# Kernel tuning notes

Measured on AMD Instinct MI355X. Metric: run time of the kernel, lower is better.

Reference implementation:

```python
import jax, jax.numpy as jnp
import numpy as np

NH = 8          # attention heads
TEMP = 2.0      # gumbel temperature


def _gumbel_softmax_hard(logits, key, temperature):
    # hard=True straight-through gumbel softmax (module is in eval mode)
    g = jax.random.gumbel(key, logits.shape, logits.dtype)
    y = jax.nn.softmax((logits + g) / temperature, axis=-1)
    y_hard = jax.nn.one_hot(jnp.argmax(y, axis=-1), logits.shape[-1], dtype=y.dtype)
    return y_hard - jax.lax.stop_gradient(y) + y


def _experts(x, w1, w2, w3):
    # SwiGLU FFN over all experts at once: x [T,C], w1/w3 [E,H,C], w2 [E,C,H] -> [T,E,C]
    h = jax.nn.silu(jnp.einsum('tc,ehc->teh', x, w1)) * jnp.einsum('tc,ehc->teh', x, w3)
    return jnp.einsum('teh,ech->tec', h, w2)


def _mha(q_in, kv_in, in_w, in_b, out_w, out_b):
    C = q_in.shape[-1]
    hd = C // NH
    q = q_in @ in_w[:C].T + in_b[:C]
    k = kv_in @ in_w[C:2 * C].T + in_b[C:2 * C]
    v = kv_in @ in_w[2 * C:].T + in_b[2 * C:]
    B, Tq, _ = q.shape
    Tk = k.shape[1]
    q = q.reshape(B, Tq, NH, hd)
    k = k.reshape(B, Tk, NH, hd)
    v = v.reshape(B, Tk, NH, hd)
    scale = jnp.asarray(1.0 / np.sqrt(hd), q.dtype)
    att = jax.nn.softmax(jnp.einsum('bqhd,bkhd->bhqk', q, k) * scale, axis=-1)
    o = jnp.einsum('bhqk,bkhd->bqhd', att, v).reshape(B, Tq, C)
    return o @ out_w.T + out_b


def setup_inputs() -> dict:
    key = jax.random.key(0)
    ks = jax.random.split(key, 20)
    B, T, S, C, E, H = 2, 2048, 77, 1024, 4, 2816
    p = lambda k, sh: jax.random.normal(k, sh, jnp.float32) * 0.02
    return {
        'x': jax.random.normal(ks[0], (B, T, C), jnp.float32),
        'time': jax.random.normal(ks[1], (B,), jnp.float32),
        'caption': jax.random.normal(ks[2], (B, S, C), jnp.float32),
        'language': jax.random.randint(ks[3], (B,), 0, 9),
        'lang_embed': p(ks[4], (9, C)),
        'lang_gate_w': p(ks[5], (E, C)),
        'lang_gate_b': jnp.zeros((E,), jnp.float32),
        'lang_w1': p(ks[6], (E, H, C)),
        'lang_w2': p(ks[7], (E, C, H)),
        'lang_w3': p(ks[8], (E, H, C)),
        'in_proj_w': p(ks[9], (3 * C, C)),
        'in_proj_b': jnp.zeros((3 * C,), jnp.float32),
        'out_proj_w': p(ks[10], (C, C)),
        'out_proj_b': jnp.zeros((C,), jnp.float32),
        'cap_gate_w': p(ks[11], (E, C)),
        'cap_gate_b': jnp.zeros((E,), jnp.float32),
        'cap_w1': p(ks[12], (E, H, C)),
        'cap_w2': p(ks[13], (E, C, H)),
        'cap_w3': p(ks[14], (E, H, C)),
    }


def reference(x, time, caption, language, lang_embed, lang_gate_w, lang_gate_b,
              lang_w1, lang_w2, lang_w3, in_proj_w, in_proj_b, out_proj_w, out_proj_b,
              cap_gate_w, cap_gate_b, cap_w1, cap_w2, cap_w3):
    B, T, C = x.shape
    x_flat = x.reshape(-1, C)                                   # [B*T, C]

    # language gating (one logit vector per batch element, repeated over T tokens)
    lang_emb = lang_embed[language]                             # [B, C]
    lang_logits = lang_emb @ lang_gate_w.T + lang_gate_b        # [B, E]
    lang_probs = _gumbel_softmax_hard(lang_logits, jax.random.key(1), TEMP)
    lang_probs = jnp.repeat(lang_probs, T, axis=0)              # [B*T, E]

    lang_outputs = _experts(x_flat, lang_w1, lang_w2, lang_w3)  # [B*T, E, C]
    first_out = (lang_outputs * lang_probs[:, :, None]).sum(axis=1)  # [B*T, C]
    first_reshaped = first_out.reshape(B, T, C)

    # cross attention against caption, then per-token caption gating
    cross = _mha(first_reshaped, caption, in_proj_w, in_proj_b, out_proj_w, out_proj_b)
    cross_flat = cross.reshape(-1, C)
    cap_logits = cross_flat @ cap_gate_w.T + cap_gate_b         # [B*T, E]
    cap_probs = _gumbel_softmax_hard(cap_logits, jax.random.key(2), TEMP)

    cap_outputs = _experts(first_out, cap_w1, cap_w2, cap_w3)   # [B*T, E, C]
    second_out = (cap_outputs * cap_probs[:, :, None]).sum(axis=1)

    total_out = (first_out + second_out).reshape(B, T, C)

    all_probs = jnp.concatenate([lang_probs, cap_probs], axis=1)  # [B*T, 2E]
    expert_usage = all_probs.mean(axis=0)
    loss = (expert_usage * jnp.log(expert_usage + 1e-10)).sum()
    return total_out, loss
```

## Files before the change

### kernel.cpp

```cpp
#include <hip/hip_runtime.h>
#include <stdint.h>

#define B_ 2
#define T_ 2048
#define S_ 77
#define C_ 1024
#define E_ 4
#define H_ 2816
#define NH_ 8
#define HD_ 128
#define N_ (B_*T_)
#define MAXGB (N_/128 + E_)
#define MAXGB2 (N_/256 + E_)
#define PEsz ((size_t)H_*C_)
#define CC_ ((size_t)C_*C_)

typedef _Float16 h8 __attribute__((ext_vector_type(8)));
typedef _Float16 h4 __attribute__((ext_vector_type(4)));
typedef float f4 __attribute__((ext_vector_type(4)));

__device__ __forceinline__ void gload16(const void* g, void* l){
  __builtin_amdgcn_global_load_lds((const __attribute__((address_space(1))) void*)g,
                                   (__attribute__((address_space(3))) void*)l, 16, 0, 0);
}

__device__ __forceinline__ uint32_t rotl32(uint32_t v, int r){ return (v<<r)|(v>>(32-r)); }
__device__ __forceinline__ void threefry2x32(uint32_t k0, uint32_t k1,
                                             uint32_t x, uint32_t y,
                                             uint32_t& o0, uint32_t& o1){
  uint32_t k2 = k0 ^ k1 ^ 0x1BD11BDAu;
  x += k0; y += k1;
#define TFR(r) { x += y; y = rotl32(y, r); y ^= x; }
  TFR(13) TFR(15) TFR(26) TFR(6)   x += k1; y += k2 + 1u;
  TFR(17) TFR(29) TFR(16) TFR(24)  x += k2; y += k0 + 2u;
  TFR(13) TFR(15) TFR(26) TFR(6)   x += k0; y += k1 + 3u;
  TFR(17) TFR(29) TFR(16) TFR(24)  x += k1; y += k2 + 4u;
  TFR(13) TFR(15) TFR(26) TFR(6)   x += k2; y += k0 + 5u;
#undef TFR
  o0 = x; o1 = y;
}
__device__ __forceinline__ float gumbel_from_bits(uint32_t bits){
  const float TINY = 1.17549435e-38f;
  float f = __uint_as_float((bits >> 9) | 0x3f800000u) - 1.0f;
  float u = fmaxf(TINY, f + TINY);
  return -logf(-logf(u));
}
__device__ __forceinline__ float jax_gumbel(uint32_t k0, uint32_t k1, uint32_t idx){
  uint32_t a, b;
  threefry2x32(k0, k1, 0u, idx, a, b);
  return gumbel_from_bits(a ^ b);
}

__device__ __forceinline__ void job_split(const float* __restrict__ s,
    _Float16* __restrict__ hi, _Float16* __restrict__ lo, long n4, long gtid, long gstride){
  for (long i = gtid; i < n4; i += gstride){
    float4 v = ((const float4*)s)[i];
    h4 h, L;
    h[0]=(_Float16)v.x; h[1]=(_Float16)v.y; h[2]=(_Float16)v.z; h[3]=(_Float16)v.w;
    L[0]=(_Float16)(v.x-(float)h[0]); L[1]=(_Float16)(v.y-(float)h[1]);
    L[2]=(_Float16)(v.z-(float)h[2]); L[3]=(_Float16)(v.w-(float)h[3]);
    ((h4*)hi)[i] = h; ((h4*)lo)[i] = L;
  }
}
__device__ __forceinline__ void job_plain(const float* __restrict__ s,
    _Float16* __restrict__ d, long n4, long gtid, long gstride){
  for (long i = gtid; i < n4; i += gstride){
    float4 v = ((const float4*)s)[i];
    h4 h;
    h[0]=(_Float16)v.x; h[1]=(_Float16)v.y; h[2]=(_Float16)v.z; h[3]=(_Float16)v.w;
    ((h4*)d)[i] = h;
  }
}
__device__ __forceinline__ void job_w13_plain(const float* __restrict__ w1,
    const float* __restrict__ w3, _Float16* __restrict__ dst, int nslot, long gtid, long gstride){
  const int K8 = C_/8;
  long total = (long)nslot * (2*H_) * K8;
  for (long i = gtid; i < total; i += gstride){
    int kv = (int)(i & (K8-1));
    long rs = i >> 7;
    int r  = (int)(rs % (2*H_));
    int slot = (int)(rs / (2*H_));
    int gg = r >> 5, o = r & 31;
    const float* src = ((o<16)? w1 : w3) + (size_t)slot*PEsz + (size_t)(16*gg + (o&15))*C_ + kv*8;
    float4 v0 = *(const float4*)src, v1 = *(const float4*)(src+4);
    float vv[8] = {v0.x,v0.y,v0.z,v0.w,v1.x,v1.y,v1.z,v1.w};
    h8 hh;
#pragma unroll
    for (int jj=0;jj<8;++jj) hh[jj] = (_Float16)vv[jj];
    *(h8*)(dst + (size_t)slot*2*PEsz + (size_t)r*C_ + kv*8) = hh;
  }
}
__device__ __forceinline__ void job_w13_split_sel(const float* __restrict__ w1,
    const float* __restrict__ w3, int sel0, int sel1,
    _Float16* __restrict__ hi, _Float16* __restrict__ lo, long gtid, long gstride){
  const int K8 = C_/8;
  long total = 2L * (2*H_) * K8;
  for (long i = gtid; i < total; i += gstride){
    int kv = (int)(i & (K8-1));
    long rs = i >> 7;
    int r  = (int)(rs % (2*H_));
    int slot = (int)(rs / (2*H_));
    int e = slot ? sel1 : sel0;
    int gg = r >> 5, o = r & 31;
    const float* src = ((o<16)? w1 : w3) + (size_t)e*PEsz + (size_t)(16*gg + (o&15))*C_ + kv*8;
    float4 v0 = *(const float4*)src, v1 = *(const float4*)(src+4);
    float vv[8] = {v0.x,v0.y,v0.z,v0.w,v1.x,v1.y,v1.z,v1.w};
    h8 hh, ll;
#pragma unroll
    for (int jj=0;jj<8;++jj){
      hh[jj] = (_Float16)vv[jj];
      ll[jj] = (_Float16)(vv[jj]-(float)hh[jj]);
    }
    size_t dof = (size_t)slot*2*PEsz + (size_t)r*C_ + kv*8;
    *(h8*)(hi + dof) = hh;
    *(h8*)(lo + dof) = ll;
  }
}
__device__ __forceinline__ void job_w2_split_sel(const float* __restrict__ w2,
    int sel0, int sel1, _Float16* __restrict__ hi, _Float16* __restrict__ lo, long gtid, long gstride){
  long per = (long)(PEsz/4);
  for (long i = gtid; i < 2*per; i += gstride){
    int slot = (i >= per) ? 1 : 0;
    long ii = i - (long)slot*per;
    float4 v = ((const float4*)(w2 + (size_t)(slot?sel1:sel0)*PEsz))[ii];
    h4 h, L;
    h[0]=(_Float16)v.x; h[1]=(_Float16)v.y; h[2]=(_Float16)v.z; h[3]=(_Float16)v.w;
    L[0]=(_Float16)(v.x-(float)h[0]); L[1]=(_Float16)(v.y-(float)h[1]);
    L[2]=(_Float16)(v.z-(float)h[2]); L[3]=(_Float16)(v.w-(float)h[3]);
    ((h4*)(hi + (size_t)slot*PEsz))[ii] = h;
    ((h4*)(lo + (size_t)slot*PEsz))[ii] = L;
  }
}
__device__ __forceinline__ void job_foldw(const float* __restrict__ outw,
    const float* __restrict__ capgw, const float* __restrict__ outb,
    float* __restrict__ Wp, float* __restrict__ bp, int b0){
  int e = b0 >> 2;
  int k = ((b0 & 3) << 8) + threadIdx.x;
  const float* cg = capgw + e*C_;
  float acc = 0.f;
  for (int c = 0; c < C_; ++c) acc += cg[c] * outw[(size_t)c*C_ + k];
  Wp[e*C_ + k] = acc;
  if ((b0 & 3) == 0){
    int wv = threadIdx.x >> 6, l = threadIdx.x & 63;
    const float* cg2 = capgw + wv*C_;
    float a2 = 0.f;
    for (int c = l; c < C_; c += 64) a2 += outb[c] * cg2[c];
#pragma unroll
    for (int off = 32; off; off >>= 1) a2 += __shfl_xor(a2, off);
    if (l == 0 && e == 0) bp[wv] = a2;
  }
}

#define CVA_W13 1024
#define CVA_W2  512
#define CVA_X   256
#define CVA_TOT (CVA_W13+CVA_W2+CVA_X)
__global__ __launch_bounds__(256) void convA(
    const float* __restrict__ lang_embed, const float* __restrict__ gate_w,
    const float* __restrict__ gate_b, const int* __restrict__ language,
    const float* __restrict__ w1, const float* __restrict__ w3, const float* __restrict__ w2,
    const float* __restrict__ x,
    _Float16* __restrict__ w13hi, _Float16* __restrict__ w13lo,
    _Float16* __restrict__ w2hi, _Float16* __restrict__ w2lo,
    _Float16* __restrict__ xhi, _Float16* __restrict__ xlo,
    float* __restrict__ langP, int* __restrict__ counts)
{
  __shared__ float lds8[8];
  const int tid = threadIdx.x, w = tid>>6, l = tid&63;
  for (int p = 2*w; p < 2*w+2; ++p){
    int b = p>>2, e = p&3;
    const float* emb = lang_embed + (size_t)language[b]*C_;
    const float* gw  = gate_w + (size_t)e*C_;
    float acc = 0.f;
    for (int c = l; c < C_; c += 64) acc += emb[c]*gw[c];
#pragma unroll
    for (int off = 32; off; off >>= 1) acc += __shfl_xor(acc, off);
    if (l == 0) lds8[p] = acc + gate_b[e];
  }
  __syncthreads();
  int sel[2];
  for (int b = 0; b < 2; ++b){
    float z[4], m = -3.4e38f;
    for (int e = 0; e < 4; ++e){
      float g = jax_gumbel(0u, 1u, (uint32_t)(b*4 + e));
      z[e] = (lds8[b*4 + e] + g) * 0.5f;
      m = fmaxf(m, z[e]);
    }
    float y[4], sum = 0.f;
    for (int e = 0; e < 4; ++e){ y[e] = expf(z[e]-m); sum += y[e]; }
    for (int e = 0; e < 4; ++e) y[e] = y[e] / sum;
    int best = 0; float bv = y[0];
    for (int e = 1; e < 4; ++e) if (y[e] > bv){ bv = y[e]; best = e; }
    sel[b] = best;
    if (blockIdx.x == 0 && tid == 0){
      for (int e = 0; e < 4; ++e)
        langP[b*4 + e] = ((e == best) ? 1.0f : 0.0f) - y[e] + y[e];
    }
  }
  if (blockIdx.x == 0 && tid == 0){
    for (int e = 0; e < 4; ++e) counts[e] = 0;
  }
  int bid = blockIdx.x;
  if (bid < CVA_W13)
    job_w13_split_sel(w1, w3, sel[0], sel[1], w13hi, w13lo,
                      (long)bid*256 + tid, (long)CVA_W13*256);
  else if (bid < CVA_W13+CVA_W2)
    job_w2_split_sel(w2, sel[0], sel[1], w2hi, w2lo,
                     (long)(bid-CVA_W13)*256 + tid, (long)CVA_W2*256);
  else
    job_split(x, xhi, xlo, (long)((size_t)N_*C_/4),
              (long)(bid-CVA_W13-CVA_W2)*256 + tid, (long)CVA_X*256);
}

#define GS_GEMM 704
#define GS_RID  640
__global__ __launch_bounds__(512) void gemm_gate_split(
    const _Float16* __restrict__ Ahi, const _Float16* __restrict__ Alo,
    const _Float16* __restrict__ Bhi, const _Float16* __restrict__ Blo,
    _Float16* __restrict__ Hhi, _Float16* __restrict__ Hlo,
    const float* __restrict__ cap_w1, const float* __restrict__ cap_w3,
    const float* __restrict__ in_w, const float* __restrict__ caption,
    const float* __restrict__ cap_w2,
    _Float16* __restrict__ capw13, _Float16* __restrict__ inwh, _Float16* __restrict__ inwl,
    _Float16* __restrict__ caph, _Float16* __restrict__ capl, _Float16* __restrict__ capw2f)
{
  __shared__ __align__(16) char smem[147456];
  const int tid = threadIdx.x;
  int bid = blockIdx.x;
  if (bid >= GS_GEMM){
    int rid = bid - GS_GEMM;
    if (rid < 352)      job_w13_plain(cap_w1, cap_w3, capw13, 4, (long)rid*512 + tid, 352L*512);
    else if (rid < 496) job_split(in_w, inwh, inwl, (long)(3*CC_/4), (long)(rid-352)*512 + tid, 144L*512);
    else if (rid < 512) job_split(caption, caph, capl, (long)((size_t)B_*S_*C_/4), (long)(rid-496)*512 + tid, 16L*512);
    else                job_plain(cap_w2, capw2f, (long)(4*PEsz/4), (long)(rid-512)*512 + tid, 128L*512);
    return;
  }
  {
    int xcd = bid & 7, idx = bid >> 3;
    bid = xcd*88 + idx;
  }
  const int bx = bid / 16, by = bid % 16;
  const int w = tid>>6, l = tid&63;
  const int lm = l&15, g = l>>4;
  const int wm = w>>1, wn = w&1;
  const int n0 = bx<<7;
  const int m0 = by<<8;
  const size_t eoff = (m0 >= T_) ? (size_t)2*PEsz : 0;

  const _Float16* srcA[4]; const _Float16* srcB[2];
#pragma unroll
  for (int jj=0;jj<4;++jj){
    int c = jj*512 + tid, r = c>>3, s = c&7;
    int st = s ^ (r&7);
    srcA[jj] = (st<4 ? Ahi : Alo) + (size_t)(m0 + r)*C_ + ((st&3)<<3);
  }
#pragma unroll
  for (int jj=0;jj<2;++jj){
    int c = jj*512 + tid, r = c>>3, s = c&7;
    int st = s ^ (r&7);
    srcB[jj] = (st<4 ? Bhi : Blo) + eoff + (size_t)(n0 + r)*C_ + ((st&3)<<3);
  }

#define STGF(ts, bi) { \
    int k0 = (ts)<<5; \
    char* db = smem + (bi)*49152; \
    _Pragma("unroll") \
    for (int jj=0;jj<4;++jj) gload16(srcA[jj]+k0, db + (jj*512 + w*64)*16); \
    _Pragma("unroll") \
    for (int jj=0;jj<2;++jj) gload16(srcB[jj]+k0, db + 32768 + (jj*512 + w*64)*16); \
  }

  const int shi = (g ^ (lm&7)) << 4;
  int aoff[4], boff[4];
#pragma unroll
  for (int i=0;i<4;++i){
    aoff[i] = ((wm*64 + i*16 + lm)<<7) + shi;
    boff[i] = 32768 + ((wn*64 + i*16 + lm)<<7) + shi;
  }

  f4 acc[4][4] = {};
  const int nt = C_/32;
  STGF(0,0) STGF(1,1)
  for (int t=0; t<nt; ++t){
    const int bi = t%3;
    const bool ds = (t+2 < nt);
    const int k2 = (t+2)<<5;
    char* db2 = smem + ((t+2)%3)*49152;
    if (t+1 < nt) { asm volatile("s_waitcnt vmcnt(6)" ::: "memory"); }
    else          { asm volatile("s_waitcnt vmcnt(0)" ::: "memory"); }
    __builtin_amdgcn_s_barrier();
    asm volatile("" ::: "memory");
    const char* base = smem + bi*49152;
    if (ds){
      gload16(srcA[0]+k2, db2 + (0*512 + w*64)*16);
      gload16(srcA[1]+k2, db2 + (1*512 + w*64)*16);
    }
    h8 ah[4], bh[4];
#pragma unroll
    for (int i=0;i<4;++i){ ah[i] = *(const h8*)(base + aoff[i]); bh[i] = *(const h8*)(base + boff[i]); }
    __builtin_amdgcn_s_setprio(1);
#pragma unroll
    for (int mi=0;mi<4;++mi)
#pragma unroll
      for (int ni=0;ni<4;++ni)
        acc[mi][ni] = __builtin_amdgcn_mfma_f32_16x16x32_f16(ah[mi], bh[ni], acc[mi][ni],0,0,0);
    __builtin_amdgcn_s_setprio(0);
    if (ds){
      gload16(srcA[2]+k2, db2 + (2*512 + w*64)*16);
      gload16(srcA[3]+k2, db2 + (3*512 + w*64)*16);
    }
    h8 bl[4];
#pragma unroll
    for (int i=0;i<4;++i) bl[i] = *(const h8*)(base + (boff[i]^64));
    __builtin_amdgcn_s_setprio(1);
#pragma unroll
    for (int mi=0;mi<4;++mi)
#pragma unroll
      for (int ni=0;ni<4;++ni)
        acc[mi][ni] = __builtin_amdgcn_mfma_f32_16x16x32_f16(ah[mi], bl[ni], acc[mi][ni],0,0,0);
    __builtin_amdgcn_s_setprio(0);
    if (ds){
      gload16(srcB[0]+k2, db2 + 32768 + (0*512 + w*64)*16);
      gload16(srcB[1]+k2, db2 + 32768 + (1*512 + w*64)*16);
    }
    h8 al[4];
#pragma unroll
    for (int i=0;i<4;++i) al[i] = *(const h8*)(base + (aoff[i]^64));
    __builtin_amdgcn_s_setprio(1);
#pragma unroll
    for (int mi=0;mi<4;++mi)
#pragma unroll
      for (int ni=0;ni<4;++ni)
        acc[mi][ni] = __builtin_amdgcn_mfma_f32_16x16x32_f16(al[mi], bh[ni], acc[mi][ni],0,0,0);
    __builtin_amdgcn_s_setprio(0);
    asm volatile("" ::: "memory");
  }
#undef STGF

#pragma unroll
  for (int mi=0;mi<4;++mi){
#pragma unroll
    for (int p=0;p<2;++p){
      int hc = ((n0 + wn*64)>>1) + p*16 + lm;
#pragma unroll
      for (int j=0;j<4;++j){
        int rl = wm*64 + mi*16 + (g<<2) + j;
        float s1 = acc[mi][2*p][j], s3 = acc[mi][2*p+1][j];
        float hval = s1/(1.f+expf(-s1))*s3;
        size_t row = (size_t)(m0 + rl);
        _Float16 hh = (_Float16)hval;
        Hhi[row*H_ + hc] = hh;
        Hlo[row*H_ + hc] = (_Float16)(hval - (float)hh);
      }
    }
  }
}

__global__ __launch_bounds__(512) void gemm_gate_plain(
    const _Float16* __restrict__ A, const _Float16* __restrict__ Bw,
    _Float16* __restrict__ Hout,
    const int* __restrict__ bmap_e, const int* __restrict__ bmap_s,
    const int* __restrict__ offs, const int* __restrict__ perm)
{
  __shared__ __align__(16) char smem[147456];
  const int tid = threadIdx.x, w = tid>>6, l = tid&63;
  const int lm = l&15, g = l>>4;
  const int wm = w>>1, wn = w&1;
  int bx = blockIdx.x, by = blockIdx.y;
  {
    int nx = gridDim.x, ny = gridDim.y;
    int nwg = nx*ny;
    int wg = by*nx + bx;
    int q = nwg >> 3, r = nwg & 7;
    int xcd = wg & 7, idx = wg >> 3;
    int s = (xcd < r ? xcd*(q+1) : r*(q+1) + (xcd-r)*q) + idx;
    bx = s / ny; by = s % ny;
  }
  const int e = bmap_e[by]; if (e<0) return;
  const int m0 = bmap_s[by];
  int v = offs[e+1]-m0; const int valid = v>256?256:v;
  const size_t eoff = (size_t)e*2*PEsz;
  const int n0 = bx<<7;

  const _Float16* srcA[4]; const _Float16* srcB[2];
#pragma unroll
  for (int jj=0;jj<4;++jj){
    int c = jj*512 + tid, r = c>>3, s = c&7;
    int st = s ^ (r&7);
    int ia = m0 + r; ia = (ia<N_) ? ia : (N_-1);
    srcA[jj] = A + (size_t)perm[ia]*C_ + (st<<3);
  }
#pragma unroll
  for (int jj=0;jj<2;++jj){
    int c = jj*512 + tid, r = c>>3, s = c&7;
    int st = s ^ (r&7);
    srcB[jj] = Bw + eoff + (size_t)(n0 + r)*C_ + (st<<3);
  }

#define STGF(ts, bi) { \
    int k0 = (ts)<<6; \
    char* db = smem + (bi)*49152; \
    _Pragma("unroll") \
    for (int jj=0;jj<4;++jj) gload16(srcA[jj]+k0, db + (jj*512 + w*64)*16); \
    _Pragma("unroll") \
    for (int jj=0;jj<2;++jj) gload16(srcB[jj]+k0, db + 32768 + (jj*512 + w*64)*16); \
  }

  const int shi = (g ^ (lm&7)) << 4;
  int aoff[4], boff[4];
#pragma unroll
  for (int i=0;i<4;++i){
    aoff[i] = ((wm*64 + i*16 + lm)<<7) + shi;
    boff[i] = 32768 + ((wn*64 + i*16 + lm)<<7) + shi;
  }

  f4 acc[4][4] = {};
  const int nt = C_/64;
  STGF(0,0) STGF(1,1)
  for (int t=0; t<nt; ++t){
    const int bi = t%3;
    const bool ds = (t+2 < nt);
    const int k2 = (t+2)<<6;
    char* db2 = smem + ((t+2)%3)*49152;
    if (t+1 < nt) { asm volatile("s_waitcnt vmcnt(6)" ::: "memory"); }
    else          { asm volatile("s_waitcnt vmcnt(0)" ::: "memory"); }
    __builtin_amdgcn_s_barrier();
    asm volatile("" ::: "memory");
    const char* base = smem + bi*49152;
#pragma unroll
    for (int kk=0;kk<2;++kk){
      if (ds){
        if (kk == 0){
          gload16(srcA[0]+k2, db2 + (0*512 + w*64)*16);
          gload16(srcA[1]+k2, db2 + (1*512 + w*64)*16);
          gload16(srcA[2]+k2, db2 + (2*512 + w*64)*16);
        } else {
          gload16(srcA[3]+k2, db2 + (3*512 + w*64)*16);
          gload16(srcB[0]+k2, db2 + 32768 + (0*512 + w*64)*16);
          gload16(srcB[1]+k2, db2 + 32768 + (1*512 + w*64)*16);
        }
      }
      h8 af[4], bf[4];
      const int x = kk<<6;
#pragma unroll
      for (int i=0;i<4;++i){ af[i] = *(const h8*)(base + (aoff[i]^x)); bf[i] = *(const h8*)(base + (boff[i]^x)); }
      __builtin_amdgcn_s_setprio(1);
#pragma unroll
      for (int mi=0;mi<4;++mi)
#pragma unroll
        for (int ni=0;ni<4;++ni)
          acc[mi][ni] = __builtin_amdgcn_mfma_f32_16x16x32_f16(af[mi], bf[ni], acc[mi][ni],0,0,0);
      __builtin_amdgcn_s_setprio(0);
    }
    asm volatile("" ::: "memory");
  }
#undef STGF

#pragma unroll
  for (int mi=0;mi<4;++mi){
#pragma unroll
    for (int p=0;p<2;++p){
      int hc = ((n0 + wn*64)>>1) + p*16 + lm;
#pragma unroll
      for (int j=0;j<4;++j){
        int rl = wm*64 + mi*16 + (g<<2) + j;
        if (rl >= valid) continue;
        float s1 = acc[mi][2*p][j], s3 = acc[mi][2*p+1][j];
        Hout[(size_t)(m0 + rl)*H_ + hc] = (_Float16)(s1/(1.f+expf(-s1))*s3);
      }
    }
  }
}

template<int EPI, int NSEG, int EXPM, int NBUF>
__device__ __forceinline__ void gemm8_body(
    char* smem,
    const _Float16* __restrict__ A0, const _Float16* __restrict__ A1,
    const _Float16* __restrict__ B0, const _Float16* __restrict__ B1,
    const float* __restrict__ bias, float* __restrict__ Cf32,
    _Float16* __restrict__ O0, _Float16* __restrict__ O1,
    const int* __restrict__ bmap_e, const int* __restrict__ bmap_s,
    const int* __restrict__ offs, const int* __restrict__ perm,
    int M, int K, int Nw, size_t bstride_e, int bx, int by)
{
  const int tid = threadIdx.x, w = tid>>6, l = tid&63;
  const int lm = l&15, g = l>>4;
  const int wm = w>>1, wn = w&1;
  const int n0 = bx<<7;
  int m0, valid = 128; size_t eoff = 0;
  if constexpr (EXPM==3){
    int e = bmap_e[by]; if (e<0) return;
    m0 = bmap_s[by];
    int v = offs[e+1]-m0; valid = v>128?128:v;
    eoff = (size_t)e*bstride_e;
  } else {
    m0 = by<<7;
    if constexpr (EXPM==1) eoff = (m0>=T_) ? bstride_e : 0;
  }
  const int cAe = (((tid&7) ^ ((tid>>3)&7)) << 3);
  size_t rbA[4], rbB[4];
#pragma unroll
  for (int j=0;j<4;++j){
    int r = (j<<5) + (tid>>3);
    int ia = m0 + r;
    if constexpr (EXPM==3){ ia = (ia < N_) ? ia : (N_-1); }
    else { if (ia > M-1) ia = M-1; }
    rbA[j] = (size_t)ia*K + cAe;
    rbB[j] = eoff + (size_t)(n0+r)*K + cAe;
  }
  const int tps = K>>6, nt = NSEG*tps;

#define SEGDEC(tt, kkv, Asrcv, Bsrcv) \
    int sg = 0; \
    if constexpr (NSEG==3){ sg = ((tt)>=2*tps) ? 2 : (((tt)>=tps)?1:0); } \
    const _Float16* Asrcv = (sg==1) ? A1 : A0; \
    const _Float16* Bsrcv = (sg==2) ? B1 : B0; \
    int kkv = ((tt) - sg*tps)<<6;

#define STG_A(tt, cc) { \
    SEGDEC(tt, kk0, Asrc, Bsrc) (void)Bsrc; \
    char* db = smem + (cc)*32768 + w*1024; \
    _Pragma("unroll") \
    for (int j=0;j<4;++j) gload16(Asrc + rbA[j] + kk0, db + j*4096); \
  }
#define STG_B(tt, cc) { \
    SEGDEC(tt, kk0, Asrc, Bsrc) (void)Asrc; \
    char* db = smem + (cc)*32768 + w*1024; \
    _Pragma("unroll") \
    for (int j=0;j<4;++j) gload16(Bsrc + rbB[j] + kk0, db + 16384 + j*4096); \
  }

  int aoff[2][4], boff[2][4];
#pragma unroll
  for (int kk=0;kk<2;++kk){
#pragma unroll
    for (int i=0;i<4;++i){
      int ra = wm*64 + i*16 + lm;
      aoff[kk][i] = (ra<<7) + (((kk<<6)+(g<<4)) ^ ((ra&7)<<4));
      int rb = wn*64 + i*16 + lm;
      boff[kk][i] = (rb<<7) + (((kk<<6)+(g<<4)) ^ ((rb&7)<<4));
    }
  }

  f4 acc[4][4] = {};
  STG_A(0,0) STG_B(0,0)
  if constexpr (NBUF==3){ STG_A(1,1) STG_B(1,1) }
  for (int t=0; t<nt; ++t){
    const int rb = t % NBUF;
    const int ts = t + NBUF - 1;
    const bool ds = ts < nt;
    const int wbuf = ts % NBUF;
    if (t+1 < nt){
      if constexpr (NBUF==3) asm volatile("s_waitcnt vmcnt(8)" ::: "memory");
      else                   asm volatile("s_waitcnt vmcnt(0)" ::: "memory");
    } else {
      asm volatile("s_waitcnt vmcnt(0)" ::: "memory");
    }
    __builtin_amdgcn_s_barrier();
    asm volatile("" ::: "memory");
    const char* Ab = smem + rb*32768;
    const char* Bb = Ab + 16384;
    if (ds) STG_A(ts, wbuf)
    {
      h8 af[4], bf[4];
#pragma unroll
      for (int i=0;i<4;++i){
        af[i] = *(const h8*)(Ab + aoff[0][i]);
        bf[i] = *(const h8*)(Bb + boff[0][i]);
      }
      __builtin_amdgcn_s_setprio(1);
#pragma unroll
      for (int mi=0;mi<4;++mi)
#pragma unroll
        for (int ni=0;ni<4;++ni)
          acc[mi][ni] = __builtin_amdgcn_mfma_f32_16x16x32_f16(af[mi], bf[ni], acc[mi][ni],0,0,0);
      __builtin_amdgcn_s_setprio(0);
    }
    if (ds) STG_B(ts, wbuf)
    {
      h8 af[4], bf[4];
#pragma unroll
      for (int i=0;i<4;++i){
        af[i] = *(const h8*)(Ab + aoff[1][i]);
        bf[i] = *(const h8*)(Bb + boff[1][i]);
      }
      __builtin_amdgcn_s_setprio(1);
#pragma unroll
      for (int mi=0;mi<4;++mi)
#pragma unroll
        for (int ni=0;ni<4;++ni)
          acc[mi][ni] = __builtin_amdgcn_mfma_f32_16x16x32_f16(af[mi], bf[ni], acc[mi][ni],0,0,0);
      __builtin_amdgcn_s_setprio(0);
    }
    asm volatile("" ::: "memory");
  }

#pragma unroll
  for (int mi=0;mi<4;++mi){
    const int rl0 = wm*64 + mi*16 + (g<<2);
#pragma unroll
    for (int ni=0;ni<4;++ni){
      int col = n0 + wn*64 + ni*16 + lm;
#pragma unroll
      for (int j=0;j<4;++j){
        int rl = rl0 + j;
        float vv = acc[mi][ni][j];
        if constexpr (EPI==1){
          int grow = m0 + rl;
          if (grow < M){
            float vb = vv + (bias ? bias[col] : 0.f);
            _Float16 hh = (_Float16)vb;
            O0[(size_t)grow*Nw + col] = hh;
            O1[(size_t)grow*Nw + col] = (_Float16)(vb - (float)hh);
          }
        } else {
          if (rl < valid){
            int orig = perm[m0 + rl];
            size_t o = (size_t)orig*C_ + col;
            Cf32[o] = (float)O0[o] + (float)O1[o] + vv;
          }
        }
      }
    }
  }
#undef STG_A
#undef STG_B
#undef SEGDEC
}

__global__ __launch_bounds__(256) void ffn1_out(
    const _Float16* __restrict__ Hbh, const _Float16* __restrict__ Hbl,
    const _Float16* __restrict__ w2hi, const _Float16* __restrict__ w2lo,
    _Float16* __restrict__ Fh, _Float16* __restrict__ Fl)
{
  __shared__ __align__(16) char smem[98304];
  int id = blockIdx.x;
  gemm8_body<1,3,1,3>(smem, Hbh, Hbl, w2hi, w2lo, nullptr, nullptr, Fh, Fl,
                      nullptr,nullptr,nullptr,nullptr, N_, H_, C_, PEsz, id&7, id>>3);
}

__global__ __launch_bounds__(256) void gemm_qkv(
    const _Float16* __restrict__ Fh, const _Float16* __restrict__ Fl,
    const _Float16* __restrict__ caph, const _Float16* __restrict__ capl,
    const _Float16* __restrict__ inwh, const _Float16* __restrict__ inwl,
    const float* __restrict__ in_b,
    _Float16* __restrict__ Qh, _Float16* __restrict__ Ql,
    _Float16* __restrict__ KVh, _Float16* __restrict__ KVl,
    const float* __restrict__ out_w, const float* __restrict__ cap_gw,
    const float* __restrict__ out_b, float* __restrict__ Wp, float* __restrict__ bp)
{
  __shared__ __align__(16) char smem[65536];
  int id = blockIdx.x;
  if (id < 256){
    gemm8_body<1,3,0,2>(smem, Fh, Fl, inwh, inwl, in_b, nullptr, Qh, Ql,
                        nullptr,nullptr,nullptr,nullptr, N_, C_, C_, 0, id&7, id>>3);
  } else if (id < 288){
    int cid = id - 256;
    gemm8_body<1,3,0,2>(smem, caph, capl, inwh + CC_, inwl + CC_, in_b + C_,
                        nullptr, KVh, KVl, nullptr,nullptr,nullptr,nullptr,
                        B_*S_, C_, 2*C_, 0, cid & 15, cid >> 4);
  } else {
    job_foldw(out_w, cap_gw, out_b, Wp, bp, id-288);
  }
}

#define SP5 5
#define KSTR 136
#define VSTR 104
__global__ __launch_bounds__(256) void attn_mfma(
    const _Float16* __restrict__ Qh, const _Float16* __restrict__ Ql,
    const _Float16* __restrict__ KVh, const _Float16* __restrict__ KVl,
    _Float16* __restrict__ AOh, _Float16* __restrict__ AOl)
{
  __shared__ __align__(16) _Float16 Usm[2*128*VSTR];
  __shared__ __align__(16) _Float16 Psm[2*64*VSTR];
  int id = blockIdx.x;
  _Float16* Kh_s = Usm;
  _Float16* Kl_s = Usm + 128*VSTR;
  _Float16* VTh  = Usm;
  _Float16* VTl  = Usm + 128*VSTR;
  _Float16* Ph   = Psm;
  _Float16* Pl   = Psm + 64*VSTR;

  const int tid = threadIdx.x;
  const int w = tid>>6, l = tid&63, lm = l&15, g = l>>4;
  const int b = id >> 8, h = (id >> 5) & 7, q0 = (id & 31) << 6;
  const float scale = 0.08838834764831845f;

  for (int i = tid; i < 64*VSTR; i += 256) ((uint32_t*)Psm)[i] = 0;
  {
    int oct = tid & 15, s0 = tid >> 4;
    for (int s = s0; s < 80; s += 16){
      h8 vh = {}, vl = {};
      if (s < S_){
        size_t ga = ((size_t)(b*S_ + s))*(2*C_) + h*HD_ + oct*8;
        vh = *(const h8*)(KVh + ga);
        vl = *(const h8*)(KVl + ga);
      }
      *(h8*)(Kh_s + s*KSTR + oct*8) = vh;
      *(h8*)(Kl_s + s*KSTR + oct*8) = vl;
    }
  }
  h8 qh[4], ql[4];
  {
    size_t qrow = (size_t)(b*T_ + q0 + w*16 + lm);
    const _Float16* qph = Qh + qrow*C_ + h*HD_ + g*8;
    const _Float16* qpl = Ql + qrow*C_ + h*HD_ + g*8;
#pragma unroll
    for (int ks=0; ks<4; ++ks){ qh[ks] = *(const h8*)(qph + ks*32); ql[ks] = *(const h8*)(qpl + ks*32); }
  }
  __syncthreads();

  f4 sc[SP5] = {};
#pragma unroll
  for (int ks=0; ks<4; ++ks){
#pragma unroll
    for (int nt=0; nt<SP5; ++nt){
      h8 kh = *(const h8*)(Kh_s + (nt*16+lm)*KSTR + ks*32 + g*8);
      h8 kl = *(const h8*)(Kl_s + (nt*16+lm)*KSTR + ks*32 + g*8);
      sc[nt] = __builtin_amdgcn_mfma_f32_16x16x32_f16(qh[ks], kh, sc[nt],0,0,0);
      sc[nt] = __builtin_amdgcn_mfma_f32_16x16x32_f16(ql[ks], kh, sc[nt],0,0,0);
      sc[nt] = __builtin_amdgcn_mfma_f32_16x16x32_f16(qh[ks], kl, sc[nt],0,0,0);
    }
  }

  float mx[4] = {-3e38f,-3e38f,-3e38f,-3e38f};
#pragma unroll
  for (int nt=0; nt<SP5; ++nt){
    bool valid = (nt*16+lm) < S_;
#pragma unroll
    for (int j=0;j<4;++j){
      float v = valid ? sc[nt][j]*scale : -3e38f;
      sc[nt][j] = v;
      mx[j] = fmaxf(mx[j], v);
    }
  }
#pragma unroll
  for (int off=1; off<16; off<<=1){
#pragma unroll
    for (int j=0;j<4;++j) mx[j] = fmaxf(mx[j], __shfl_xor(mx[j], off));
  }
  float sm[4] = {0,0,0,0};
#pragma unroll
  for (int nt=0; nt<SP5; ++nt){
    bool valid = (nt*16+lm) < S_;
#pragma unroll
    for (int j=0;j<4;++j){
      float p = valid ? expf(sc[nt][j]-mx[j]) : 0.f;
      sc[nt][j] = p; sm[j] += p;
    }
  }
#pragma unroll
  for (int off=1; off<16; off<<=1){
#pragma unroll
    for (int j=0;j<4;++j) sm[j] += __shfl_xor(sm[j], off);
  }
#pragma unroll
  for (int nt=0; nt<SP5; ++nt){
#pragma unroll
    for (int j=0;j<4;++j){
      int col = nt*16 + lm;
      if (col < S_){
        float p = sc[nt][j] / sm[j];
        int row = w*16 + g*4 + j;
        _Float16 ph = (_Float16)p;
        Ph[row*VSTR + col] = ph;
        Pl[row*VSTR + col] = (_Float16)(p - (float)ph);
      }
    }
  }
  __syncthreads();

  for (int i = tid; i < 128*VSTR; i += 256) ((uint32_t*)Usm)[i] = 0;
  __syncthreads();
  {
    int oct = tid & 15, s0 = tid >> 4;
    for (int s = s0; s < S_; s += 16){
      size_t ga = ((size_t)(b*S_ + s))*(2*C_) + C_ + h*HD_ + oct*8;
      h8 vh = *(const h8*)(KVh + ga);
      h8 vl = *(const h8*)(KVl + ga);
#pragma unroll
      for (int i2=0;i2<8;++i2){
        VTh[(oct*8+i2)*VSTR + s] = vh[i2];
        VTl[(oct*8+i2)*VSTR + s] = vl[i2];
      }
    }
  }
  __syncthreads();

  h8 pah[3], pal[3];
#pragma unroll
  for (int ks=0;ks<3;++ks){
    pah[ks] = *(const h8*)(Ph + (w*16+lm)*VSTR + ks*32 + g*8);
    pal[ks] = *(const h8*)(Pl + (w*16+lm)*VSTR + ks*32 + g*8);
  }
#pragma unroll
  for (int nt=0; nt<8; ++nt){
    f4 o = {};
#pragma unroll
    for (int ks=0;ks<3;++ks){
      h8 vh = *(const h8*)(VTh + (nt*16+lm)*VSTR + ks*32 + g*8);
      h8 vl = *(const h8*)(VTl + (nt*16+lm)*VSTR + ks*32 + g*8);
      o = __builtin_amdgcn_mfma_f32_16x16x32_f16(pah[ks], vh, o,0,0,0);
      o = __builtin_amdgcn_mfma_f32_16x16x32_f16(pal[ks], vh, o,0,0,0);
      o = __builtin_amdgcn_mfma_f32_16x16x32_f16(pah[ks], vl, o,0,0,0);
    }
#pragma unroll
    for (int j=0;j<4;++j){
      size_t orow = (size_t)(b*T_ + q0 + w*16 + g*4 + j);
      size_t oa = orow*C_ + h*HD_ + nt*16 + lm;
      _Float16 hh = (_Float16)o[j];
      AOh[oa] = hh;
      AOl[oa] = (_Float16)(o[j] - (float)hh);
    }
  }
}

__global__ __launch_bounds__(256) void cap_gate(
    const _Float16* __restrict__ AOh, const _Float16* __restrict__ AOl,
    const float* __restrict__ Wp, const float* __restrict__ bp,
    const float* __restrict__ gb,
    int* __restrict__ cap_sel, float* __restrict__ capP, int* __restrict__ counts)
{
  int tid = threadIdx.x, wave = tid >> 6, lane = tid & 63;
  for (int r = 0; r < 2; ++r){
    int row = (blockIdx.x << 3) + (wave << 1) + r;
    float av[16];
#pragma unroll
    for (int i = 0; i < 16; ++i){
      int c = lane + (i << 6);
      av[i] = (float)AOh[(size_t)row*C_ + c] + (float)AOl[(size_t)row*C_ + c];
    }
    float lg[E_];
#pragma unroll
    for (int e = 0; e < E_; ++e){
      const float* wv = Wp + (size_t)e * C_;
      float p = 0.f;
#pragma unroll
      for (int i = 0; i < 16; ++i) p += av[i] * wv[lane + (i << 6)];
#pragma unroll
      for (int off = 32; off; off >>= 1) p += __shfl_xor(p, off);
      lg[e] = p + bp[e] + gb[e];
    }
    if (lane == 0){
      float z[E_], m = -3.4e38f;
      for (int e = 0; e < E_; ++e){
        float gmb = jax_gumbel(0u, 2u, (uint32_t)(row*E_ + e));
        z[e] = (lg[e] + gmb) * 0.5f;
        m = fmaxf(m, z[e]);
      }
      float y[E_], sum = 0.f;
      for (int e = 0; e < E_; ++e){ y[e] = expf(z[e] - m); sum += y[e]; }
      for (int e = 0; e < E_; ++e) y[e] = y[e] / sum;
      int best = 0; float bv = y[0];
      for (int e = 1; e < E_; ++e) if (y[e] > bv){ bv = y[e]; best = e; }
      cap_sel[row] = best;
      atomicAdd(&counts[best], 1);
      for (int e = 0; e < E_; ++e)
        capP[(size_t)row*E_ + e] = ((e == best) ? 1.0f : 0.0f) - y[e] + y[e];
    }
  }
}

__global__ __launch_bounds__(256) void finalize(
    const int* __restrict__ counts, const int* __restrict__ cap_sel,
    int* __restrict__ offs,
    int* __restrict__ bmap_e, int* __restrict__ bmap_s,
    int* __restrict__ bmap_e2, int* __restrict__ bmap_s2,
    int* __restrict__ perm,
    const float* __restrict__ capP, const float* __restrict__ langP,
    float* __restrict__ out_loss)
{
  __shared__ int loffs[5];
  __shared__ int lcur[4];
  __shared__ float red[4][256];
  int tid = threadIdx.x;
  if (blockIdx.x == 0){
    if (tid == 0){
      loffs[0] = 0;
      for (int e = 0; e < E_; ++e){ loffs[e+1] = loffs[e] + counts[e]; lcur[e] = loffs[e]; }
      for (int e = 0; e < E_+1; ++e) offs[e] = loffs[e];
      int idx = 0;
      for (int e = 0; e < E_; ++e)
        for (int s = loffs[e]; s < loffs[e+1]; s += 128){ bmap_e[idx] = e; bmap_s[idx] = s; ++idx; }
      for (; idx < MAXGB; ++idx) bmap_e[idx] = -1;
      int idx2 = 0;
      for (int e = 0; e < E_; ++e)
        for (int s = loffs[e]; s < loffs[e+1]; s += 256){ bmap_e2[idx2] = e; bmap_s2[idx2] = s; ++idx2; }
      for (; idx2 < MAXGB2; ++idx2) bmap_e2[idx2] = -1;
    }
    __syncthreads();
    for (int row = tid; row < N_; row += 256){
      int e = cap_sel[row];
      int pos = atomicAdd(&lcur[e], 1);
      perm[pos] = row;
    }
  } else {
    float p0=0.f, p1=0.f, p2=0.f, p3=0.f;
    for (int r = tid; r < N_; r += 256){
      const float* p = capP + (size_t)r*E_;
      p0 += p[0]; p1 += p[1]; p2 += p[2]; p3 += p[3];
    }
    red[0][tid]=p0; red[1][tid]=p1; red[2][tid]=p2; red[3][tid]=p3;
    __syncthreads();
    for (int s = 128; s > 0; s >>= 1){
      if (tid < s){
        red[0][tid]+=red[0][tid+s]; red[1][tid]+=red[1][tid+s];
        red[2][tid]+=red[2][tid+s]; red[3][tid]+=red[3][tid+s];
      }
      __syncthreads();
    }
    if (tid == 0){
      float loss = 0.f;
      for (int e = 0; e < E_; ++e){
        float ul = (langP[e] + langP[E_ + e]) * 0.5f;
        loss += ul * logf(ul + 1e-10f);
      }
      for (int e = 0; e < E_; ++e){
        float uc = red[e][0] * (1.0f / N_);
        loss += uc * logf(uc + 1e-10f);
      }
      out_loss[0] = loss;
    }
  }
}

__global__ __launch_bounds__(256) void ffn2_out(
    const _Float16* __restrict__ H2, const _Float16* __restrict__ capw2f,
    float* __restrict__ out,
    const _Float16* __restrict__ Fh, const _Float16* __restrict__ Fl,
    const int* __restrict__ bmap_e, const int* __restrict__ bmap_s,
    const int* __restrict__ offs, const int* __restrict__ perm)
{
  __shared__ __align__(16) char smem[65536];
  int bx = blockIdx.x, by = blockIdx.y;
  {
    int nx = gridDim.x, ny = gridDim.y;
    int nwg = nx*ny;
    int wg = by*nx + bx;
    int q = nwg >> 3, r = nwg & 7;
    int xcd = wg & 7, idx = wg >> 3;
    int s = (xcd < r ? xcd*(q+1) : r*(q+1) + (xcd-r)*q) + idx;
    bx = s / ny; by = s % ny;
  }
  gemm8_body<2,1,3,2>(smem, H2, nullptr, capw2f, nullptr, nullptr, out,
                      (_Float16*)Fh, (_Float16*)Fl,
                      bmap_e, bmap_s, offs, perm, N_, H_, C_, PEsz, bx, by);
}

extern "C" void kernel_launch(void* const* d_in, const int* in_sizes, int n_in,
                              void* d_out, int out_size, void* d_ws, size_t ws_size,
                              hipStream_t stream)
{
  const float* x          = (const float*)d_in[0];
  const float* caption    = (const float*)d_in[2];
  const int*   language   = (const int*)  d_in[3];
  const float* lang_embed = (const float*)d_in[4];
  const float* lang_gw    = (const float*)d_in[5];
  const float* lang_gb    = (const float*)d_in[6];
  const float* lang_w1    = (const float*)d_in[7];
  const float* lang_w2    = (const float*)d_in[8];
  const float* lang_w3    = (const float*)d_in[9];
  const float* in_w       = (const float*)d_in[10];
  const float* in_b       = (const float*)d_in[11];
  const float* out_w      = (const float*)d_in[12];
  const float* out_b      = (const float*)d_in[13];
  const float* cap_gw     = (const float*)d_in[14];
  const float* cap_gb     = (const float*)d_in[15];
  const float* cap_w1     = (const float*)d_in[16];
  const float* cap_w2     = (const float*)d_in[17];
  const float* cap_w3     = (const float*)d_in[18];
  float* out = (float*)d_out;

  const size_t NC = (size_t)N_*C_;
  const size_t NHe = (size_t)N_*H_;
  const size_t KVel = (size_t)B_*S_*2*C_;
  const size_t CAPel = (size_t)B_*S_*C_;

  char* base = (char*)d_ws;
  size_t cur = 0;
  auto alloc = [&](size_t bytes)->char*{
    char* p = base + cur;
    cur += (bytes + 255) & ~(size_t)255;
    return p;
  };
  _Float16* Qh = (_Float16*)alloc(NC*2);
  _Float16* Ql = (_Float16*)alloc(NC*2);
  char* kvreg = alloc(KVel*4);
  _Float16* KVh = (_Float16*)kvreg;
  _Float16* KVl = KVh + KVel;
  float* capP   = (float*)alloc((size_t)N_*E_*4);
  float* langP  = (float*)alloc(64);
  float* Wp     = (float*)alloc(E_*C_*4);
  float* bp     = (float*)alloc(64);
  int* cap_sel  = (int*)alloc(N_*4);
  int* counts   = (int*)alloc(64);
  int* offs     = (int*)alloc(64);
  int* bmap_e   = (int*)alloc(MAXGB*4);
  int* bmap_s   = (int*)alloc(MAXGB*4);
  int* bmap_e2  = (int*)alloc(MAXGB2*4);
  int* bmap_s2  = (int*)alloc(MAXGB2*4);
  int* perm     = (int*)alloc(N_*4);
  _Float16* xAO_hi = (_Float16*)alloc(NC*2);
  _Float16* xAO_lo = (_Float16*)alloc(NC*2);
  _Float16* cap_hi = (_Float16*)alloc(CAPel*2);
  _Float16* cap_lo = (_Float16*)alloc(CAPel*2);
  _Float16* Hb_hi  = (_Float16*)alloc(NHe*2);
  _Float16* Hb_lo  = (_Float16*)alloc(NHe*2);
  _Float16* F_hi   = (_Float16*)alloc(NC*2);
  _Float16* F_lo   = (_Float16*)alloc(NC*2);
  _Float16* Wreg = (_Float16*)alloc(2*( (size_t)3*CC_*2 + CC_*2 + 3*4*PEsz ));
  _Float16* w13hi = Wreg;
  _Float16* w13lo = Wreg + 4*PEsz;
  _Float16* w2hi  = Wreg + 8*PEsz;
  _Float16* w2lo  = Wreg + 10*PEsz;
  _Float16* inw_hi  = Wreg + 12*PEsz;
  _Float16* inw_lo  = inw_hi + 3*CC_;
  _Float16* capw13f = Wreg + 12*PEsz + 6*CC_;
  _Float16* capw2f  = capw13f + 8*PEsz;

  convA<<<CVA_TOT, 256, 0, stream>>>(
      lang_embed, lang_gw, lang_gb, language,
      lang_w1, lang_w3, lang_w2, x,
      w13hi, w13lo, w2hi, w2lo, xAO_hi, xAO_lo, langP, counts);

  gemm_gate_split<<<GS_GEMM + GS_RID, 512, 0, stream>>>(
      xAO_hi, xAO_lo, w13hi, w13lo, Hb_hi, Hb_lo,
      cap_w1, cap_w3, in_w, caption, cap_w2,
      capw13f, inw_hi, inw_lo, cap_hi, cap_lo, capw2f);

  ffn1_out<<<256, 256, 0, stream>>>(Hb_hi, Hb_lo, w2hi, w2lo, F_hi, F_lo);

  gemm_qkv<<<304, 256, 0, stream>>>(
      F_hi, F_lo, cap_hi, cap_lo, inw_hi, inw_lo, in_b,
      Qh, Ql, KVh, KVl, out_w, cap_gw, out_b, Wp, bp);

  attn_mfma<<<512, 256, 0, stream>>>(Qh, Ql, KVh, KVl, xAO_hi, xAO_lo);

  cap_gate<<<N_/8, 256, 0, stream>>>(xAO_hi, xAO_lo, Wp, bp, cap_gb, cap_sel, capP, counts);

  finalize<<<2, 256, 0, stream>>>(counts, cap_sel, offs, bmap_e, bmap_s,
                                  bmap_e2, bmap_s2, perm, capP, langP, out + NC);

  _Float16* H2 = Hb_hi;
  gemm_gate_plain<<<dim3((2*H_)/128, MAXGB2), 512, 0, stream>>>(
      F_hi, capw13f, H2, bmap_e2, bmap_s2, offs, perm);

  ffn2_out<<<dim3(C_/128, MAXGB), 256, 0, stream>>>(
      H2, capw2f, out, F_hi, F_lo, bmap_e, bmap_s, offs, perm);
}
```

Measured before the change: 647.8 us.

## Redistribute weight-conversion side jobs across kernels to fill idle CUs

```diff
diff --git a/kernel.cpp b/kernel.cpp
--- a/kernel.cpp
+++ b/kernel.cpp
@@ -154,15 +154,20 @@
 #define CVA_W13 1024
 #define CVA_W2  512
 #define CVA_X   256
-#define CVA_TOT (CVA_W13+CVA_W2+CVA_X)
+#define CVA_INW 96
+#define CVA_CAP 16
+#define CVA_TOT (CVA_W13+CVA_W2+CVA_X+CVA_INW+CVA_CAP)
 __global__ __launch_bounds__(256) void convA(
     const float* __restrict__ lang_embed, const float* __restrict__ gate_w,
     const float* __restrict__ gate_b, const int* __restrict__ language,
     const float* __restrict__ w1, const float* __restrict__ w3, const float* __restrict__ w2,
     const float* __restrict__ x,
+    const float* __restrict__ in_w, const float* __restrict__ caption,
     _Float16* __restrict__ w13hi, _Float16* __restrict__ w13lo,
     _Float16* __restrict__ w2hi, _Float16* __restrict__ w2lo,
     _Float16* __restrict__ xhi, _Float16* __restrict__ xlo,
+    _Float16* __restrict__ inwh, _Float16* __restrict__ inwl,
+    _Float16* __restrict__ caph, _Float16* __restrict__ capl,
     float* __restrict__ langP, int* __restrict__ counts)
 {
   __shared__ float lds8[8];
@@ -207,34 +212,25 @@
   else if (bid < CVA_W13+CVA_W2)
     job_w2_split_sel(w2, sel[0], sel[1], w2hi, w2lo,
                      (long)(bid-CVA_W13)*256 + tid, (long)CVA_W2*256);
-  else
+  else if (bid < CVA_W13+CVA_W2+CVA_X)
     job_split(x, xhi, xlo, (long)((size_t)N_*C_/4),
               (long)(bid-CVA_W13-CVA_W2)*256 + tid, (long)CVA_X*256);
-}
-
-#define GS_GEMM 704
-#define GS_RID  640
+  else if (bid < CVA_W13+CVA_W2+CVA_X+CVA_INW)
+    job_split(in_w, inwh, inwl, (long)(3*CC_/4),
+              (long)(bid-CVA_W13-CVA_W2-CVA_X)*256 + tid, (long)CVA_INW*256);
+  else
+    job_split(caption, caph, capl, (long)((size_t)B_*S_*C_/4),
+              (long)(bid-CVA_W13-CVA_W2-CVA_X-CVA_INW)*256 + tid, (long)CVA_CAP*256);
+}
+
 __global__ __launch_bounds__(512) void gemm_gate_split(
     const _Float16* __restrict__ Ahi, const _Float16* __restrict__ Alo,
     const _Float16* __restrict__ Bhi, const _Float16* __restrict__ Blo,
-    _Float16* __restrict__ Hhi, _Float16* __restrict__ Hlo,
-    const float* __restrict__ cap_w1, const float* __restrict__ cap_w3,
-    const float* __restrict__ in_w, const float* __restrict__ caption,
-    const float* __restrict__ cap_w2,
-    _Float16* __restrict__ capw13, _Float16* __restrict__ inwh, _Float16* __restrict__ inwl,
-    _Float16* __restrict__ caph, _Float16* __restrict__ capl, _Float16* __restrict__ capw2f)
+    _Float16* __restrict__ Hhi, _Float16* __restrict__ Hlo)
 {
   __shared__ __align__(16) char smem[147456];
   const int tid = threadIdx.x;
   int bid = blockIdx.x;
-  if (bid >= GS_GEMM){
-    int rid = bid - GS_GEMM;
-    if (rid < 352)      job_w13_plain(cap_w1, cap_w3, capw13, 4, (long)rid*512 + tid, 352L*512);
-    else if (rid < 496) job_split(in_w, inwh, inwl, (long)(3*CC_/4), (long)(rid-352)*512 + tid, 144L*512);
-    else if (rid < 512) job_split(caption, caph, capl, (long)((size_t)B_*S_*C_/4), (long)(rid-496)*512 + tid, 16L*512);
-    else                job_plain(cap_w2, capw2f, (long)(4*PEsz/4), (long)(rid-512)*512 + tid, 128L*512);
-    return;
-  }
   {
     int xcd = bid & 7, idx = bid >> 3;
     bid = xcd*88 + idx;
@@ -647,7 +643,9 @@
     _Float16* __restrict__ Qh, _Float16* __restrict__ Ql,
     _Float16* __restrict__ KVh, _Float16* __restrict__ KVl,
     const float* __restrict__ out_w, const float* __restrict__ cap_gw,
-    const float* __restrict__ out_b, float* __restrict__ Wp, float* __restrict__ bp)
+    const float* __restrict__ out_b, float* __restrict__ Wp, float* __restrict__ bp,
+    const float* __restrict__ cap_w1, const float* __restrict__ cap_w3,
+    _Float16* __restrict__ capw13)
 {
   __shared__ __align__(16) char smem[65536];
   int id = blockIdx.x;
@@ -659,22 +657,29 @@
     gemm8_body<1,3,0,2>(smem, caph, capl, inwh + CC_, inwl + CC_, in_b + C_,
                         nullptr, KVh, KVl, nullptr,nullptr,nullptr,nullptr,
                         B_*S_, C_, 2*C_, 0, cid & 15, cid >> 4);
+  } else if (id < 304){
+    job_foldw(out_w, cap_gw, out_b, Wp, bp, id-288);
   } else {
-    job_foldw(out_w, cap_gw, out_b, Wp, bp, id-288);
+    job_w13_plain(cap_w1, cap_w3, capw13, 4, (long)(id-304)*256 + threadIdx.x, 208L*256);
   }
 }
 
 #define SP5 5
 #define KSTR 136
 #define VSTR 104
-__global__ __launch_bounds__(256) void attn_mfma(
+__global__ __launch_bounds__(256) void attn_fused(
     const _Float16* __restrict__ Qh, const _Float16* __restrict__ Ql,
     const _Float16* __restrict__ KVh, const _Float16* __restrict__ KVl,
-    _Float16* __restrict__ AOh, _Float16* __restrict__ AOl)
+    _Float16* __restrict__ AOh, _Float16* __restrict__ AOl,
+    const float* __restrict__ cap_w2, _Float16* __restrict__ capw2f)
 {
   __shared__ __align__(16) _Float16 Usm[2*128*VSTR];
   __shared__ __align__(16) _Float16 Psm[2*64*VSTR];
   int id = blockIdx.x;
+  if (id >= 512){
+    job_plain(cap_w2, capw2f, (long)(4*PEsz/4), (long)(id-512)*256 + threadIdx.x, 128L*256);
+    return;
+  }
   _Float16* Kh_s = Usm;
   _Float16* Kl_s = Usm + 128*VSTR;
   _Float16* VTh  = Usm;
@@ -1021,21 +1026,21 @@
 
   convA<<<CVA_TOT, 256, 0, stream>>>(
       lang_embed, lang_gw, lang_gb, language,
-      lang_w1, lang_w3, lang_w2, x,
-      w13hi, w13lo, w2hi, w2lo, xAO_hi, xAO_lo, langP, counts);
-
-  gemm_gate_split<<<GS_GEMM + GS_RID, 512, 0, stream>>>(
-      xAO_hi, xAO_lo, w13hi, w13lo, Hb_hi, Hb_lo,
-      cap_w1, cap_w3, in_w, caption, cap_w2,
-      capw13f, inw_hi, inw_lo, cap_hi, cap_lo, capw2f);
+      lang_w1, lang_w3, lang_w2, x, in_w, caption,
+      w13hi, w13lo, w2hi, w2lo, xAO_hi, xAO_lo,
+      inw_hi, inw_lo, cap_hi, cap_lo, langP, counts);
+
+  gemm_gate_split<<<704, 512, 0, stream>>>(
+      xAO_hi, xAO_lo, w13hi, w13lo, Hb_hi, Hb_lo);
 
   ffn1_out<<<256, 256, 0, stream>>>(Hb_hi, Hb_lo, w2hi, w2lo, F_hi, F_lo);
 
-  gemm_qkv<<<304, 256, 0, stream>>>(
+  gemm_qkv<<<512, 256, 0, stream>>>(
       F_hi, F_lo, cap_hi, cap_lo, inw_hi, inw_lo, in_b,
-      Qh, Ql, KVh, KVl, out_w, cap_gw, out_b, Wp, bp);
-
-  attn_mfma<<<512, 256, 0, stream>>>(Qh, Ql, KVh, KVl, xAO_hi, xAO_lo);
+      Qh, Ql, KVh, KVl, out_w, cap_gw, out_b, Wp, bp,
+      cap_w1, cap_w3, capw13f);
+
+  attn_fused<<<640, 256, 0, stream>>>(Qh, Ql, KVh, KVl, xAO_hi, xAO_lo, cap_w2, capw2f);
 
   cap_gate<<<N_/8, 256, 0, stream>>>(xAO_hi, xAO_lo, Wp, bp, cap_gb, cap_sel, capP, counts);
 
```

Result: no change. 658.1 us (+1.6%).
